# Kernel tuning notes

Hardware: AMD Instinct MI355X
Metric: run time of the kernel (lower is better)

## Reference

```python
import math
import jax, jax.numpy as jnp
import numpy as np

CLUSTER_RATIO1 = 0.0625
CLUSTER_RATIO2 = 0.35
K_LAYER1 = 8
K_LAYER2 = 3


def _dpc_knn(x, cluster_num, k, key):
    """Density-peak clustering with KNN density. x: [B,N,C] -> idx_cluster [B,N]."""
    B, N, C = x.shape
    sq = jnp.sum(x * x, axis=-1)  # [B,N]
    d2 = sq[:, :, None] + sq[:, None, :] - 2.0 * jnp.einsum('bnc,bmc->bnm', x, x)
    dist = jnp.sqrt(jnp.maximum(d2, 0.0)) / jnp.sqrt(jnp.asarray(C, x.dtype))  # cdist / C**0.5
    # k nearest (smallest) distances
    neg_dn, _ = jax.lax.top_k(-dist, k)
    dist_nearest = -neg_dn  # [B,N,k]
    density = jnp.exp(-jnp.mean(dist_nearest ** 2, axis=-1))
    density = density + jax.random.uniform(key, density.shape, dtype=density.dtype) * 1e-6
    mask = (density[:, None, :] > density[:, :, None]).astype(x.dtype)  # [B,N,N]
    dist_max = jnp.max(dist.reshape(B, -1), axis=-1)[:, None, None]
    parent_dist = jnp.min(dist * mask + dist_max * (1.0 - mask), axis=-1)  # [B,N]
    score = parent_dist * density
    _, index_down = jax.lax.top_k(score, cluster_num)  # [B,cluster_num] cluster centers
    # assign each token to nearest center
    dm = jnp.take_along_axis(dist, index_down[:, :, None], axis=1)  # [B,cluster_num,N]
    idx_cluster = jnp.argmin(dm, axis=1)  # [B,N]
    bidx = jnp.arange(B)[:, None]
    idx_cluster = idx_cluster.at[bidx, index_down].set(
        jnp.broadcast_to(jnp.arange(cluster_num)[None, :], index_down.shape))
    return idx_cluster


def _merge_tokens(x, idx_cluster, cluster_num):
    """Weighted (uniform) scatter-mean of tokens into clusters. x: [B,N,C]."""
    B, N, C = x.shape
    flat = (idx_cluster + jnp.arange(B)[:, None] * cluster_num).reshape(-1)  # [B*N]
    ones = jnp.ones((B * N,), x.dtype)
    all_w = jax.ops.segment_sum(ones, flat, num_segments=B * cluster_num) + 1e-6
    norm_w = 1.0 / all_w[flat]  # token_weight == 1
    merged = jax.ops.segment_sum(x.reshape(B * N, C) * norm_w[:, None], flat,
                                 num_segments=B * cluster_num)
    return merged.reshape(B, cluster_num, C)


def _group(meta1, meta2, idx_cluster2, score_w, score_b):
    """Reorder [meta2[v]; members of cluster v from meta1] per cluster, scaled by modulation."""
    T, K1, C = meta1.shape
    K2 = meta2.shape[1]
    modu = jax.nn.softmax(meta2.mean(axis=2) @ score_w.T + score_b, axis=-1)  # [T,K2]
    # composite sort key: (cluster_id, 0 for meta2 center, 1+i for meta1 member i) -> stable grouping
    cid = jnp.concatenate([jnp.broadcast_to(jnp.arange(K2)[None, :], (T, K2)),
                           idx_cluster2], axis=1)  # [T,K2+K1]
    pos = jnp.concatenate([jnp.zeros((T, K2), jnp.int32),
                           jnp.broadcast_to(jnp.arange(1, K1 + 1, dtype=jnp.int32)[None, :], (T, K1))],
                          axis=1)
    sort_key = cid * (K1 + 2) + pos
    order = jnp.argsort(sort_key, axis=1)  # stable; keys are unique anyway
    tokens = jnp.concatenate([meta2, meta1], axis=1)  # [T,K2+K1,C]
    sorted_tokens = jnp.take_along_axis(tokens, order[:, :, None], axis=1)
    sorted_cid = jnp.take_along_axis(cid, order, axis=1)
    scale = jnp.take_along_axis(modu, sorted_cid, axis=1)  # [T,K2+K1]
    return sorted_tokens * scale[:, :, None]


def setup_inputs() -> dict:
    key = jax.random.key(0)
    k1, k2, k3 = jax.random.split(key, 3)
    T, N, C = 128, 256, 1408
    vis_embed = jax.random.normal(k1, (T, N, C), dtype=jnp.float32)
    score_w = jax.random.normal(k2, (6, 6), dtype=jnp.float32) * 0.1
    score_b = jax.random.normal(k3, (6,), dtype=jnp.float32) * 0.1
    return {"vis_embed": vis_embed, "score_w": score_w, "score_b": score_b}


def reference(vis_embed, score_w, score_b):
    T, N, C = vis_embed.shape
    cn1 = max(math.ceil(N * CLUSTER_RATIO1), 1)      # 16
    cn2 = max(math.ceil(cn1 * CLUSTER_RATIO2), 1)    # 6
    nk = jax.random.split(jax.random.key(42), 2)
    idx1 = _dpc_knn(vis_embed, cn1, K_LAYER1, nk[0])
    meta1 = _merge_tokens(vis_embed, idx1, cn1)       # [T,16,C]
    idx2 = _dpc_knn(meta1, cn2, K_LAYER2, nk[1])
    meta2 = _merge_tokens(meta1, idx2, cn2)           # [T,6,C]
    return _group(meta1, meta2, idx2, score_w, score_b)  # [T,22,C]
```

## Files before the change

### kernel.cpp

```cpp
#include <hip/hip_runtime.h>
#include <math.h>

#define T_BATCH 128
#define N_TOK   256
#define C_DIM   1408
#define CN1     16
#define KNN1    8
#define CN2     6
#define KNN2    3
#define NOUT    22
#define LS      44

typedef __attribute__((ext_vector_type(4))) short sh4;
typedef __attribute__((ext_vector_type(8))) short sh8;
typedef __attribute__((ext_vector_type(4))) float f32x4;

union frag_u { sh4 h[2]; sh8 v; };

__device__ inline sh8 ld_frag(const short* p) {
    frag_u u;
    u.h[0] = *(const sh4*)p;
    u.h[1] = *(const sh4*)(p + 4);
    return u.v;
}

__device__ inline void split2(float v0, float v1, unsigned& hip, unsigned& lop) {
    unsigned u0 = __float_as_uint(v0);
    unsigned u1 = __float_as_uint(v1);
    hip = (u0 >> 16) | (u1 & 0xFFFF0000u);
    float l0 = v0 - __uint_as_float(u0 & 0xFFFF0000u);
    float l1 = v1 - __uint_as_float(u1 & 0xFFFF0000u);
    unsigned w0 = __float_as_uint(l0);
    unsigned w1 = __float_as_uint(l1);
    w0 = w0 + 0x7FFFu + ((w0 >> 16) & 1u);
    w1 = w1 + 0x7FFFu + ((w1 >> 16) & 1u);
    lop = (w0 >> 16) | (w1 & 0xFFFF0000u);
}

#define INS8(m, v) {                                   \
    float _x = (v);                                    \
    _Pragma("unroll")                                  \
    for (int _q = 0; _q < 8; _q++) {                   \
        float _lo = fminf(m[_q], _x);                  \
        _x = fmaxf(m[_q], _x);                         \
        m[_q] = _lo;                                   \
    }                                                  \
}

__global__ __launch_bounds__(256, 4) void gemm_dist_sym(const float* __restrict__ x,
                                                        float* __restrict__ dist) {
    const int t = blockIdx.y;
    const int p = blockIdx.x;
    const int bi = (p < 4) ? 0 : (p < 7) ? 1 : (p < 9) ? 2 : 3;
    const int bj = (p < 4) ? p : (p < 7) ? p - 3 : (p < 9) ? p - 5 : 3;
    const int i0 = bi * 64, j0 = bj * 64;
    const bool diag = (bi == bj);
    const float* X = x + (size_t)t * N_TOK * C_DIM;

    __shared__ short Ahi[64 * LS], Alo[64 * LS], Bhi[64 * LS], Blo[64 * LS];
    __shared__ float nred[512];
    __shared__ float snA[64], snB[64];

    const int tid  = threadIdx.x;
    const int wave = tid >> 6;
    const int lane = tid & 63;
    const int qr   = wave >> 1;
    const int qc   = wave & 1;
    const int srow = tid >> 2;
    const int sq   = tid & 3;
    const int fr   = lane & 15;
    const int fq   = lane >> 4;

    const short* BhiS = diag ? Ahi : Bhi;
    const short* BloS = diag ? Alo : Blo;

    f32x4 acc[2][2];
#pragma unroll
    for (int a = 0; a < 2; a++)
#pragma unroll
        for (int b = 0; b < 2; b++) acc[a][b] = (f32x4){0.f, 0.f, 0.f, 0.f};

    const float* Arow = X + (size_t)(i0 + srow) * C_DIM + sq * 8;
    const float* Brow = X + (size_t)(j0 + srow) * C_DIM + sq * 8;
    float nA = 0.f, nB = 0.f;

    for (int k0 = 0; k0 < C_DIM; k0 += 32) {
        float av[8], bv[8];
        float4 a0 = *(const float4*)(Arow + k0);
        float4 a1 = *(const float4*)(Arow + k0 + 4);
        av[0] = a0.x; av[1] = a0.y; av[2] = a0.z; av[3] = a0.w;
        av[4] = a1.x; av[5] = a1.y; av[6] = a1.z; av[7] = a1.w;
#pragma unroll
        for (int e = 0; e < 8; e++) nA += av[e] * av[e];
        unsigned ah[4], al[4], bh[4], bl[4];
#pragma unroll
        for (int q = 0; q < 4; q++) split2(av[2 * q], av[2 * q + 1], ah[q], al[q]);
        if (!diag) {
            float4 b0 = *(const float4*)(Brow + k0);
            float4 b1 = *(const float4*)(Brow + k0 + 4);
            bv[0] = b0.x; bv[1] = b0.y; bv[2] = b0.z; bv[3] = b0.w;
            bv[4] = b1.x; bv[5] = b1.y; bv[6] = b1.z; bv[7] = b1.w;
#pragma unroll
            for (int e = 0; e < 8; e++) nB += bv[e] * bv[e];
#pragma unroll
            for (int q = 0; q < 4; q++) split2(bv[2 * q], bv[2 * q + 1], bh[q], bl[q]);
        }
        __syncthreads();
        {
            unsigned* AH = (unsigned*)&Ahi[srow * LS + sq * 8];
            unsigned* AL = (unsigned*)&Alo[srow * LS + sq * 8];
#pragma unroll
            for (int q = 0; q < 4; q++) { AH[q] = ah[q]; AL[q] = al[q]; }
            if (!diag) {
                unsigned* BH = (unsigned*)&Bhi[srow * LS + sq * 8];
                unsigned* BL = (unsigned*)&Blo[srow * LS + sq * 8];
#pragma unroll
                for (int q = 0; q < 4; q++) { BH[q] = bh[q]; BL[q] = bl[q]; }
            }
        }
        __syncthreads();

        sh8 fAh[2], fAl[2], fBh[2], fBl[2];
#pragma unroll
        for (int mt = 0; mt < 2; mt++) {
            int ro = (qr * 32 + mt * 16 + fr) * LS + fq * 8;
            fAh[mt] = ld_frag(&Ahi[ro]);
            fAl[mt] = ld_frag(&Alo[ro]);
            int co = (qc * 32 + mt * 16 + fr) * LS + fq * 8;
            fBh[mt] = ld_frag(&BhiS[co]);
            fBl[mt] = ld_frag(&BloS[co]);
        }
#pragma unroll
        for (int mt = 0; mt < 2; mt++)
#pragma unroll
            for (int nt = 0; nt < 2; nt++) {
                acc[mt][nt] = __builtin_amdgcn_mfma_f32_16x16x32_bf16(fAh[mt], fBh[nt], acc[mt][nt], 0, 0, 0);
                acc[mt][nt] = __builtin_amdgcn_mfma_f32_16x16x32_bf16(fAh[mt], fBl[nt], acc[mt][nt], 0, 0, 0);
                acc[mt][nt] = __builtin_amdgcn_mfma_f32_16x16x32_bf16(fAl[mt], fBh[nt], acc[mt][nt], 0, 0, 0);
            }
    }

    nred[tid] = nA;
    nred[256 + tid] = diag ? nA : nB;
    __syncthreads();
    if (tid < 64) {
        snA[tid] = nred[4 * tid] + nred[4 * tid + 1] + nred[4 * tid + 2] + nred[4 * tid + 3];
        snB[tid] = nred[256 + 4 * tid] + nred[256 + 4 * tid + 1]
                 + nred[256 + 4 * tid + 2] + nred[256 + 4 * tid + 3];
    }
    __syncthreads();

    const float inv_sqrtC = 1.0f / sqrtf((float)C_DIM);
    float* Dt = dist + (size_t)t * N_TOK * N_TOK;
#pragma unroll
    for (int mt = 0; mt < 2; mt++)
#pragma unroll
        for (int nt = 0; nt < 2; nt++) {
            int jl = qc * 32 + nt * 16 + fr;
            int jg = j0 + jl;
            float sqj = snB[jl];
            int il0 = qr * 32 + mt * 16 + fq * 4;
            float vv[4];
#pragma unroll
            for (int r = 0; r < 4; r++) {
                int ig = i0 + il0 + r;
                float d2 = snA[il0 + r] + sqj - 2.0f * acc[mt][nt][r];
                float v = (ig == jg) ? 0.0f : sqrtf(fmaxf(d2, 0.0f)) * inv_sqrtC;
                Dt[(size_t)ig * N_TOK + jg] = v;
                vv[r] = v;
            }
            if (!diag) {
                float4 o; o.x = vv[0]; o.y = vv[1]; o.z = vv[2]; o.w = vv[3];
                *(float4*)&Dt[(size_t)jg * N_TOK + i0 + il0] = o;
            }
        }
}

__global__ __launch_bounds__(512) void dpc1_fused(const float* __restrict__ dist,
                                                  int* __restrict__ memb,
                                                  int* __restrict__ cntg,
                                                  int* __restrict__ offg) {
    const int t   = blockIdx.x;
    const int tid = threadIdx.x;
    const int col = tid & 255;
    const int h   = tid >> 8;
    const float* D = dist + (size_t)t * N_TOK * N_TOK;

    __shared__ float dens_s[N_TOK];
    __shared__ float red[512];
    __shared__ float lists[KNN1][520];
    __shared__ unsigned long long wbest[8];
    __shared__ int centers[CN1];
    __shared__ int bks[N_TOK];
    __shared__ int cnt_s[CN1], off_s[CN1];

    float c0[8], c1[8], c2[8], c3[8];
#pragma unroll
    for (int q = 0; q < 8; q++) { c0[q] = 3.4e38f; c1[q] = 3.4e38f; c2[q] = 3.4e38f; c3[q] = 3.4e38f; }
    float mx = 0.f;
    const float* base = D + (size_t)(h * 128) * N_TOK + col;
    for (int jj = 0; jj < 128; jj += 4) {
        float d0 = base[(size_t)(jj + 0) * N_TOK];
        float d1 = base[(size_t)(jj + 1) * N_TOK];
        float d2 = base[(size_t)(jj + 2) * N_TOK];
        float d3 = base[(size_t)(jj + 3) * N_TOK];
        mx = fmaxf(mx, fmaxf(fmaxf(d0, d1), fmaxf(d2, d3)));
        INS8(c0, d0); INS8(c1, d1); INS8(c2, d2); INS8(c3, d3);
    }
#pragma unroll
    for (int q = 0; q < 8; q++) { INS8(c0, c1[q]); }
#pragma unroll
    for (int q = 0; q < 8; q++) { INS8(c0, c2[q]); }
#pragma unroll
    for (int q = 0; q < 8; q++) { INS8(c0, c3[q]); }
#pragma unroll
    for (int q = 0; q < 8; q++) lists[q][tid] = c0[q];
    red[tid] = mx;
    __syncthreads();
#pragma unroll
    for (int s = 256; s > 0; s >>= 1) {
        if (tid < s) red[tid] = fmaxf(red[tid], red[tid + s]);
        __syncthreads();
    }
    const float dmax = red[0];
    __syncthreads();

    if (h == 0) {
#pragma unroll
        for (int q = 0; q < 8; q++) { float v = lists[q][col + 256]; INS8(c0, v); }
        float s2 = 0.f;
#pragma unroll
        for (int q = 0; q < 8; q++) s2 += c0[q] * c0[q];
        dens_s[col] = expf(-s2 / (float)KNN1);
    }
    __syncthreads();
    const float dens = dens_s[col];

    float p0 = dmax, p1 = dmax, p2 = dmax, p3 = dmax;
    const float* dsh = dens_s + h * 128;
    for (int jj = 0; jj < 128; jj += 4) {
        float d0 = base[(size_t)(jj + 0) * N_TOK];
        float d1 = base[(size_t)(jj + 1) * N_TOK];
        float d2 = base[(size_t)(jj + 2) * N_TOK];
        float d3 = base[(size_t)(jj + 3) * N_TOK];
        p0 = (dsh[jj + 0] > dens) ? fminf(p0, d0) : p0;
        p1 = (dsh[jj + 1] > dens) ? fminf(p1, d1) : p1;
        p2 = (dsh[jj + 2] > dens) ? fminf(p2, d2) : p2;
        p3 = (dsh[jj + 3] > dens) ? fminf(p3, d3) : p3;
    }
    red[tid] = fminf(fminf(p0, p1), fminf(p2, p3));
    __syncthreads();
    float score = 0.f;
    if (h == 0) score = fminf(red[col], red[col + 256]) * dens;

    unsigned long long key = 0;
    if (h == 0)
        key = ((unsigned long long)__float_as_uint(score) << 32) | (unsigned)(65535 - col);
    for (int k = 0; k < CN1; k++) {
        unsigned long long mm = key;
#pragma unroll
        for (int off = 32; off > 0; off >>= 1) {
            unsigned long long o = __shfl_xor(mm, off);
            mm = (o > mm) ? o : mm;
        }
        if ((tid & 63) == 0) wbest[tid >> 6] = mm;
        __syncthreads();
        unsigned long long b = wbest[0];
#pragma unroll
        for (int w = 1; w < 8; w++) b = (wbest[w] > b) ? wbest[w] : b;
        int idx = 65535 - (int)(b & 0xFFFFull);
        if (tid == 0) centers[k] = idx;
        if (tid == idx) key = 0;
        __syncthreads();
    }

    int bk = 0;
    if (h == 0) {
        float bd = 3.4e38f;
#pragma unroll
        for (int k = 0; k < CN1; k++) {
            float d = D[(size_t)centers[k] * N_TOK + col];
            if (d < bd) { bd = d; bk = k; }
        }
#pragma unroll
        for (int k = 0; k < CN1; k++) if (col == centers[k]) bk = k;
        bks[col] = bk;
    }
    __syncthreads();
    if (tid < CN1) {
        int c = 0;
        for (int j = 0; j < N_TOK; j++) c += (bks[j] == tid);
        cnt_s[tid] = c;
    }
    __syncthreads();
    if (tid == 0) {
        int o = 0;
        for (int q = 0; q < CN1; q++) { off_s[q] = o; o += cnt_s[q]; }
    }
    __syncthreads();
    if (h == 0) {
        int rank = 0;
        for (int j = 0; j < col; j++) rank += (bks[j] == bk);
        memb[t * N_TOK + off_s[bk] + rank] = col;
    }
    if (tid < CN1) {
        cntg[t * CN1 + tid] = cnt_s[tid];
        offg[t * CN1 + tid] = off_s[tid];
    }
}

__global__ __launch_bounds__(256) void merge1_kernel(const float* __restrict__ x,
                                                     const int* __restrict__ memb,
                                                     const int* __restrict__ cntg,
                                                     const int* __restrict__ offg,
                                                     float* __restrict__ meta1) {
    const int q   = blockIdx.x;
    const int t   = blockIdx.y;
    const int tid = threadIdx.x;
    const int n    = cntg[t * CN1 + q];
    const int base = t * N_TOK + offg[t * CN1 + q];
    const int c0 = tid, c1 = tid + 256;
    const bool act1 = (c1 < C_DIM / 4);

    float a0x = 0.f, a0y = 0.f, a0z = 0.f, a0w = 0.f;
    float a1x = 0.f, a1y = 0.f, a1z = 0.f, a1w = 0.f;
    for (int m = 0; m < n; m++) {
        int row = memb[base + m];
        const float4* xr = (const float4*)(x + ((size_t)t * N_TOK + row) * C_DIM);
        float4 v0 = xr[c0];
        a0x += v0.x; a0y += v0.y; a0z += v0.z; a0w += v0.w;
        if (act1) {
            float4 v1 = xr[c1];
            a1x += v1.x; a1y += v1.y; a1z += v1.z; a1w += v1.w;
        }
    }
    float w = 1.0f / ((float)n + 1e-6f);
    float4* mr = (float4*)(meta1 + ((size_t)t * CN1 + q) * C_DIM);
    float4 o0; o0.x = a0x * w; o0.y = a0y * w; o0.z = a0z * w; o0.w = a0w * w;
    mr[c0] = o0;
    if (act1) {
        float4 o1; o1.x = a1x * w; o1.y = a1y * w; o1.z = a1z * w; o1.w = a1w * w;
        mr[c1] = o1;
    }
}

__global__ __launch_bounds__(256) void layer2_kernel(const float* __restrict__ meta1,
                                                     const float* __restrict__ score_w,
                                                     const float* __restrict__ score_b,
                                                     float* __restrict__ out) {
    const int t   = blockIdx.x;
    const int tid = threadIdx.x;
    const float* M = meta1 + (size_t)t * CN1 * C_DIM;

    __shared__ float buf[CN1][132];
    __shared__ float d2s[CN1][CN1];
    __shared__ float m2[CN2][C_DIM];
    __shared__ float dens[CN1], scor[CN1], nrm[CN1], rmx[CN1];
    __shared__ int   centers[CN2], idx2s[CN1], cnt2[CN2];
    __shared__ float modu[CN2], msum[CN2];
    __shared__ int   srcRow[NOUT], cidArr[NOUT];
    __shared__ float dmax_sh;

    const int ti = tid >> 4;
    const int tj = tid & 15;

    float acc = 0.f;
    for (int c0 = 0; c0 < C_DIM; c0 += 128) {
        for (int e = tid; e < CN1 * 128; e += 256) {
            int r = e >> 7, c = e & 127;
            buf[r][c] = M[(size_t)r * C_DIM + c0 + c];
        }
        __syncthreads();
#pragma unroll
        for (int cc = 0; cc < 128; cc += 4) {
            float4 a = *(const float4*)&buf[ti][cc];
            float4 b = *(const float4*)&buf[tj][cc];
            acc += a.x * b.x + a.y * b.y + a.z * b.z + a.w * b.w;
        }
        __syncthreads();
    }
    if (ti == tj) nrm[ti] = acc;
    __syncthreads();

    const float inv_sqrtC = 1.0f / sqrtf((float)C_DIM);
    {
        float d2 = nrm[ti] + nrm[tj] - 2.f * acc;
        d2s[ti][tj] = sqrtf(fmaxf(d2, 0.f)) * inv_sqrtC;
    }
    __syncthreads();

    if (tid < CN1) {
        float m0 = 3.4e38f, m1 = 3.4e38f, m2v = 3.4e38f, mx = 0.f;
        for (int j = 0; j < CN1; j++) {
            float d = d2s[tid][j];
            mx = fmaxf(mx, d);
            if (d < m2v) {
                m2v = d;
                if (m2v < m1) { float tmp = m2v; m2v = m1; m1 = tmp; }
                if (m1 < m0)  { float tmp = m1;  m1 = m0;  m0 = tmp; }
            }
        }
        dens[tid] = expf(-(m0 * m0 + m1 * m1 + m2v * m2v) / (float)KNN2);
        rmx[tid] = mx;
    }
    __syncthreads();
    if (tid == 0) {
        float g = 0.f;
        for (int j = 0; j < CN1; j++) g = fmaxf(g, rmx[j]);
        dmax_sh = g;
    }
    __syncthreads();

    if (tid < CN1) {
        float di = dens[tid];
        float pd = dmax_sh;
        for (int j = 0; j < CN1; j++)
            if (dens[j] > di) pd = fminf(pd, d2s[tid][j]);
        scor[tid] = pd * di;
    }
    __syncthreads();

    if (tid == 0) {
        for (int k = 0; k < CN2; k++) {
            float best = -3.4e38f; int bi = 0;
            for (int j = 0; j < CN1; j++)
                if (scor[j] > best) { best = scor[j]; bi = j; }
            centers[k] = bi;
            scor[bi] = -3.4e38f;
        }
    }
    __syncthreads();

    if (tid < CN1) {
        float bd = 3.4e38f; int bk = 0;
#pragma unroll
        for (int k = 0; k < CN2; k++) {
            float d = d2s[centers[k]][tid];
            if (d < bd) { bd = d; bk = k; }
        }
#pragma unroll
        for (int k = 0; k < CN2; k++) if (tid == centers[k]) bk = k;
        idx2s[tid] = bk;
    }
    __syncthreads();

    if (tid == 0) {
        for (int v = 0; v < CN2; v++) cnt2[v] = 0;
        for (int i = 0; i < CN1; i++) cnt2[idx2s[i]]++;
        int slot = 0;
        for (int v = 0; v < CN2; v++) {
            srcRow[slot] = CN1 + v; cidArr[slot] = v; slot++;
            for (int i = 0; i < CN1; i++)
                if (idx2s[i] == v) { srcRow[slot] = i; cidArr[slot] = v; slot++; }
        }
        for (int v = 0; v < CN2; v++) msum[v] = 0.f;
    }
    __syncthreads();

    float ls[CN2] = {0.f, 0.f, 0.f, 0.f, 0.f, 0.f};
    for (int ch = tid; ch < C_DIM; ch += 256) {
        float a6[CN2] = {0.f, 0.f, 0.f, 0.f, 0.f, 0.f};
        for (int r = 0; r < CN1; r++) {
            float v = M[(size_t)r * C_DIM + ch];
            int c = idx2s[r];
#pragma unroll
            for (int q = 0; q < CN2; q++) a6[q] += (c == q) ? v : 0.f;
        }
#pragma unroll
        for (int q = 0; q < CN2; q++) {
            float mv = a6[q] / ((float)cnt2[q] + 1e-6f);
            m2[q][ch] = mv;
            ls[q] += mv;
        }
    }
#pragma unroll
    for (int q = 0; q < CN2; q++) atomicAdd(&msum[q], ls[q]);
    __syncthreads();

    if (tid == 0) {
        float mean[CN2], lg[CN2];
        for (int v = 0; v < CN2; v++) mean[v] = msum[v] / (float)C_DIM;
        float mxl = -3.4e38f;
        for (int u = 0; u < CN2; u++) {
            float s = score_b[u];
            for (int v = 0; v < CN2; v++) s += mean[v] * score_w[u * CN2 + v];
            lg[u] = s;
            mxl = fmaxf(mxl, s);
        }
        float den = 0.f;
        for (int u = 0; u < CN2; u++) { lg[u] = expf(lg[u] - mxl); den += lg[u]; }
        for (int u = 0; u < CN2; u++) modu[u] = lg[u] / den;
    }
    __syncthreads();

    float* ob = out + (size_t)t * NOUT * C_DIM;
    for (int ch = tid; ch < C_DIM; ch += 256) {
#pragma unroll
        for (int s = 0; s < NOUT; s++) {
            int r = srcRow[s];
            float v = (r < CN1) ? M[(size_t)r * C_DIM + ch] : m2[r - CN1][ch];
            ob[(size_t)s * C_DIM + ch] = v * modu[cidArr[s]];
        }
    }
}

extern "C" void kernel_launch(void* const* d_in, const int* in_sizes, int n_in,
                              void* d_out, int out_size, void* d_ws, size_t ws_size,
                              hipStream_t stream) {
    const float* x  = (const float*)d_in[0];
    const float* sw = (const float*)d_in[1];
    const float* sb = (const float*)d_in[2];
    float* out = (float*)d_out;

    float* ws     = (float*)d_ws;
    float* dist   = ws;
    float* meta1  = dist + (size_t)T_BATCH * N_TOK * N_TOK;
    int*   memb   = (int*)(meta1 + (size_t)T_BATCH * CN1 * C_DIM);
    int*   cntg   = memb + (size_t)T_BATCH * N_TOK;
    int*   offg   = cntg + T_BATCH * CN1;

    gemm_dist_sym<<<dim3(10, T_BATCH), 256, 0, stream>>>(x, dist);
    dpc1_fused<<<T_BATCH, 512, 0, stream>>>(dist, memb, cntg, offg);
    merge1_kernel<<<dim3(CN1, T_BATCH), 256, 0, stream>>>(x, memb, cntg, offg, meta1);
    layer2_kernel<<<T_BATCH, 256, 0, stream>>>(meta1, sw, sb, out);
}
```

Baseline: 443.9 us.

## Remap GEMM block order, widen DPC and layer2 blocks, unroll merge gather

```diff
diff --git a/kernel.cpp b/kernel.cpp
--- a/kernel.cpp
+++ b/kernel.cpp
@@ -49,8 +49,12 @@
 
 __global__ __launch_bounds__(256, 4) void gemm_dist_sym(const float* __restrict__ x,
                                                         float* __restrict__ dist) {
-    const int t = blockIdx.y;
-    const int p = blockIdx.x;
+    const int id = blockIdx.x;
+    const int r  = id & 7;
+    const int q8 = id >> 3;
+    const int p  = q8 % 10;
+    const int tt = q8 / 10;
+    const int t  = tt * 8 + r;
     const int bi = (p < 4) ? 0 : (p < 7) ? 1 : (p < 9) ? 2 : 3;
     const int bj = (p < 4) ? p : (p < 7) ? p - 3 : (p < 9) ? p - 5 : 3;
     const int i0 = bi * 64, j0 = bj * 64;
@@ -162,12 +166,12 @@
             int il0 = qr * 32 + mt * 16 + fq * 4;
             float vv[4];
 #pragma unroll
-            for (int r = 0; r < 4; r++) {
-                int ig = i0 + il0 + r;
-                float d2 = snA[il0 + r] + sqj - 2.0f * acc[mt][nt][r];
+            for (int rr = 0; rr < 4; rr++) {
+                int ig = i0 + il0 + rr;
+                float d2 = snA[il0 + rr] + sqj - 2.0f * acc[mt][nt][rr];
                 float v = (ig == jg) ? 0.0f : sqrtf(fmaxf(d2, 0.0f)) * inv_sqrtC;
                 Dt[(size_t)ig * N_TOK + jg] = v;
-                vv[r] = v;
+                vv[rr] = v;
             }
             if (!diag) {
                 float4 o; o.x = vv[0]; o.y = vv[1]; o.z = vv[2]; o.w = vv[3];
@@ -176,58 +180,55 @@
         }
 }
 
-__global__ __launch_bounds__(512) void dpc1_fused(const float* __restrict__ dist,
-                                                  int* __restrict__ memb,
-                                                  int* __restrict__ cntg,
-                                                  int* __restrict__ offg) {
-    const int t   = blockIdx.x;
-    const int tid = threadIdx.x;
-    const int col = tid & 255;
-    const int h   = tid >> 8;
+__global__ __launch_bounds__(1024) void dpc1_fused(const float* __restrict__ dist,
+                                                   int* __restrict__ memb,
+                                                   int* __restrict__ cntg,
+                                                   int* __restrict__ offg) {
+    const int t    = blockIdx.x;
+    const int tid  = threadIdx.x;
+    const int col  = tid & 255;
+    const int h    = tid >> 8;
+    const int lane = tid & 63;
+    const int wid  = tid >> 6;
     const float* D = dist + (size_t)t * N_TOK * N_TOK;
 
     __shared__ float dens_s[N_TOK];
-    __shared__ float red[512];
-    __shared__ float lists[KNN1][520];
-    __shared__ unsigned long long wbest[8];
+    __shared__ float lists[KNN1][1024];
+    __shared__ float red[1024];
+    __shared__ float rmax16[16];
+    __shared__ unsigned long long wred[16];
     __shared__ int centers[CN1];
     __shared__ int bks[N_TOK];
     __shared__ int cnt_s[CN1], off_s[CN1];
 
-    float c0[8], c1[8], c2[8], c3[8];
-#pragma unroll
-    for (int q = 0; q < 8; q++) { c0[q] = 3.4e38f; c1[q] = 3.4e38f; c2[q] = 3.4e38f; c3[q] = 3.4e38f; }
+    float c0[8], c1[8];
+#pragma unroll
+    for (int q = 0; q < 8; q++) { c0[q] = 3.4e38f; c1[q] = 3.4e38f; }
     float mx = 0.f;
-    const float* base = D + (size_t)(h * 128) * N_TOK + col;
-    for (int jj = 0; jj < 128; jj += 4) {
+    const float* base = D + (size_t)(h * 64) * N_TOK + col;
+    for (int jj = 0; jj < 64; jj += 2) {
         float d0 = base[(size_t)(jj + 0) * N_TOK];
         float d1 = base[(size_t)(jj + 1) * N_TOK];
-        float d2 = base[(size_t)(jj + 2) * N_TOK];
-        float d3 = base[(size_t)(jj + 3) * N_TOK];
-        mx = fmaxf(mx, fmaxf(fmaxf(d0, d1), fmaxf(d2, d3)));
-        INS8(c0, d0); INS8(c1, d1); INS8(c2, d2); INS8(c3, d3);
+        mx = fmaxf(mx, fmaxf(d0, d1));
+        INS8(c0, d0); INS8(c1, d1);
     }
 #pragma unroll
     for (int q = 0; q < 8; q++) { INS8(c0, c1[q]); }
 #pragma unroll
-    for (int q = 0; q < 8; q++) { INS8(c0, c2[q]); }
-#pragma unroll
-    for (int q = 0; q < 8; q++) { INS8(c0, c3[q]); }
-#pragma unroll
     for (int q = 0; q < 8; q++) lists[q][tid] = c0[q];
-    red[tid] = mx;
-    __syncthreads();
-#pragma unroll
-    for (int s = 256; s > 0; s >>= 1) {
-        if (tid < s) red[tid] = fmaxf(red[tid], red[tid + s]);
-        __syncthreads();
-    }
-    const float dmax = red[0];
-    __syncthreads();
+#pragma unroll
+    for (int off = 32; off > 0; off >>= 1) mx = fmaxf(mx, __shfl_xor(mx, off));
+    if (lane == 0) rmax16[wid] = mx;
+    __syncthreads();
+    float dmax = rmax16[0];
+#pragma unroll
+    for (int w = 1; w < 16; w++) dmax = fmaxf(dmax, rmax16[w]);
 
     if (h == 0) {
 #pragma unroll
-        for (int q = 0; q < 8; q++) { float v = lists[q][col + 256]; INS8(c0, v); }
+        for (int s = 1; s < 4; s++)
+#pragma unroll
+            for (int q = 0; q < 8; q++) { float v = lists[q][col + s * 256]; INS8(c0, v); }
         float s2 = 0.f;
 #pragma unroll
         for (int q = 0; q < 8; q++) s2 += c0[q] * c0[q];
@@ -236,22 +237,20 @@
     __syncthreads();
     const float dens = dens_s[col];
 
-    float p0 = dmax, p1 = dmax, p2 = dmax, p3 = dmax;
-    const float* dsh = dens_s + h * 128;
-    for (int jj = 0; jj < 128; jj += 4) {
+    float p0 = dmax, p1 = dmax;
+    const float* dsh = dens_s + h * 64;
+    for (int jj = 0; jj < 64; jj += 2) {
         float d0 = base[(size_t)(jj + 0) * N_TOK];
         float d1 = base[(size_t)(jj + 1) * N_TOK];
-        float d2 = base[(size_t)(jj + 2) * N_TOK];
-        float d3 = base[(size_t)(jj + 3) * N_TOK];
         p0 = (dsh[jj + 0] > dens) ? fminf(p0, d0) : p0;
         p1 = (dsh[jj + 1] > dens) ? fminf(p1, d1) : p1;
-        p2 = (dsh[jj + 2] > dens) ? fminf(p2, d2) : p2;
-        p3 = (dsh[jj + 3] > dens) ? fminf(p3, d3) : p3;
-    }
-    red[tid] = fminf(fminf(p0, p1), fminf(p2, p3));
+    }
+    red[tid] = fminf(p0, p1);
     __syncthreads();
     float score = 0.f;
-    if (h == 0) score = fminf(red[col], red[col + 256]) * dens;
+    if (h == 0)
+        score = fminf(fminf(red[col], red[col + 256]),
+                      fminf(red[col + 512], red[col + 768])) * dens;
 
     unsigned long long key = 0;
     if (h == 0)
@@ -263,11 +262,11 @@
             unsigned long long o = __shfl_xor(mm, off);
             mm = (o > mm) ? o : mm;
         }
-        if ((tid & 63) == 0) wbest[tid >> 6] = mm;
+        if (lane == 0) wred[wid] = mm;
         __syncthreads();
-        unsigned long long b = wbest[0];
-#pragma unroll
-        for (int w = 1; w < 8; w++) b = (wbest[w] > b) ? wbest[w] : b;
+        unsigned long long b = wred[0];
+#pragma unroll
+        for (int w = 1; w < 16; w++) b = (wred[w] > b) ? wred[w] : b;
         int idx = 65535 - (int)(b & 0xFFFFull);
         if (tid == 0) centers[k] = idx;
         if (tid == idx) key = 0;
@@ -321,33 +320,59 @@
     const int base = t * N_TOK + offg[t * CN1 + q];
     const int c0 = tid, c1 = tid + 256;
     const bool act1 = (c1 < C_DIM / 4);
-
-    float a0x = 0.f, a0y = 0.f, a0z = 0.f, a0w = 0.f;
-    float a1x = 0.f, a1y = 0.f, a1z = 0.f, a1w = 0.f;
-    for (int m = 0; m < n; m++) {
-        int row = memb[base + m];
-        const float4* xr = (const float4*)(x + ((size_t)t * N_TOK + row) * C_DIM);
-        float4 v0 = xr[c0];
-        a0x += v0.x; a0y += v0.y; a0z += v0.z; a0w += v0.w;
+    const float4* xb = (const float4*)(x + (size_t)t * N_TOK * C_DIM);
+    const int stride4 = C_DIM / 4;
+
+    float4 s0 = {0.f, 0.f, 0.f, 0.f};
+    float4 s1 = {0.f, 0.f, 0.f, 0.f};
+    int m = 0;
+    for (; m + 4 <= n; m += 4) {
+        int r0 = memb[base + m + 0];
+        int r1 = memb[base + m + 1];
+        int r2 = memb[base + m + 2];
+        int r3 = memb[base + m + 3];
+        float4 a0 = xb[(size_t)r0 * stride4 + c0];
+        float4 a1 = xb[(size_t)r1 * stride4 + c0];
+        float4 a2 = xb[(size_t)r2 * stride4 + c0];
+        float4 a3 = xb[(size_t)r3 * stride4 + c0];
+        s0.x += a0.x; s0.y += a0.y; s0.z += a0.z; s0.w += a0.w;
+        s0.x += a1.x; s0.y += a1.y; s0.z += a1.z; s0.w += a1.w;
+        s0.x += a2.x; s0.y += a2.y; s0.z += a2.z; s0.w += a2.w;
+        s0.x += a3.x; s0.y += a3.y; s0.z += a3.z; s0.w += a3.w;
         if (act1) {
-            float4 v1 = xr[c1];
-            a1x += v1.x; a1y += v1.y; a1z += v1.z; a1w += v1.w;
+            float4 b0 = xb[(size_t)r0 * stride4 + c1];
+            float4 b1 = xb[(size_t)r1 * stride4 + c1];
+            float4 b2 = xb[(size_t)r2 * stride4 + c1];
+            float4 b3 = xb[(size_t)r3 * stride4 + c1];
+            s1.x += b0.x; s1.y += b0.y; s1.z += b0.z; s1.w += b0.w;
+            s1.x += b1.x; s1.y += b1.y; s1.z += b1.z; s1.w += b1.w;
+            s1.x += b2.x; s1.y += b2.y; s1.z += b2.z; s1.w += b2.w;
+            s1.x += b3.x; s1.y += b3.y; s1.z += b3.z; s1.w += b3.w;
+        }
+    }
+    for (; m < n; m++) {
+        int r0 = memb[base + m];
+        float4 a0 = xb[(size_t)r0 * stride4 + c0];
+        s0.x += a0.x; s0.y += a0.y; s0.z += a0.z; s0.w += a0.w;
+        if (act1) {
+            float4 b0 = xb[(size_t)r0 * stride4 + c1];
+            s1.x += b0.x; s1.y += b0.y; s1.z += b0.z; s1.w += b0.w;
         }
     }
     float w = 1.0f / ((float)n + 1e-6f);
     float4* mr = (float4*)(meta1 + ((size_t)t * CN1 + q) * C_DIM);
-    float4 o0; o0.x = a0x * w; o0.y = a0y * w; o0.z = a0z * w; o0.w = a0w * w;
+    float4 o0; o0.x = s0.x * w; o0.y = s0.y * w; o0.z = s0.z * w; o0.w = s0.w * w;
     mr[c0] = o0;
     if (act1) {
-        float4 o1; o1.x = a1x * w; o1.y = a1y * w; o1.z = a1z * w; o1.w = a1w * w;
+        float4 o1; o1.x = s1.x * w; o1.y = s1.y * w; o1.z = s1.z * w; o1.w = s1.w * w;
         mr[c1] = o1;
     }
 }
 
-__global__ __launch_bounds__(256) void layer2_kernel(const float* __restrict__ meta1,
-                                                     const float* __restrict__ score_w,
-                                                     const float* __restrict__ score_b,
-                                                     float* __restrict__ out) {
+__global__ __launch_bounds__(1024) void layer2_kernel(const float* __restrict__ meta1,
+                                                      const float* __restrict__ score_w,
+                                                      const float* __restrict__ score_b,
+                                                      float* __restrict__ out) {
     const int t   = blockIdx.x;
     const int tid = threadIdx.x;
     const float* M = meta1 + (size_t)t * CN1 * C_DIM;
@@ -361,29 +386,31 @@
     __shared__ int   srcRow[NOUT], cidArr[NOUT];
     __shared__ float dmax_sh;
 
-    const int ti = tid >> 4;
+    const int ti = (tid < 256) ? (tid >> 4) : 0;
     const int tj = tid & 15;
 
     float acc = 0.f;
     for (int c0 = 0; c0 < C_DIM; c0 += 128) {
-        for (int e = tid; e < CN1 * 128; e += 256) {
+        for (int e = tid; e < CN1 * 128; e += 1024) {
             int r = e >> 7, c = e & 127;
             buf[r][c] = M[(size_t)r * C_DIM + c0 + c];
         }
         __syncthreads();
-#pragma unroll
-        for (int cc = 0; cc < 128; cc += 4) {
-            float4 a = *(const float4*)&buf[ti][cc];
-            float4 b = *(const float4*)&buf[tj][cc];
-            acc += a.x * b.x + a.y * b.y + a.z * b.z + a.w * b.w;
+        if (tid < 256) {
+#pragma unroll
+            for (int cc = 0; cc < 128; cc += 4) {
+                float4 a = *(const float4*)&buf[ti][cc];
+                float4 b = *(const float4*)&buf[tj][cc];
+                acc += a.x * b.x + a.y * b.y + a.z * b.z + a.w * b.w;
+            }
         }
         __syncthreads();
     }
-    if (ti == tj) nrm[ti] = acc;
+    if (tid < 256 && ti == tj) nrm[ti] = acc;
     __syncthreads();
 
     const float inv_sqrtC = 1.0f / sqrtf((float)C_DIM);
-    {
+    if (tid < 256) {
         float d2 = nrm[ti] + nrm[tj] - 2.f * acc;
         d2s[ti][tj] = sqrtf(fmaxf(d2, 0.f)) * inv_sqrtC;
     }
@@ -458,7 +485,7 @@
     __syncthreads();
 
     float ls[CN2] = {0.f, 0.f, 0.f, 0.f, 0.f, 0.f};
-    for (int ch = tid; ch < C_DIM; ch += 256) {
+    for (int ch = tid; ch < C_DIM; ch += 1024) {
         float a6[CN2] = {0.f, 0.f, 0.f, 0.f, 0.f, 0.f};
         for (int r = 0; r < CN1; r++) {
             float v = M[(size_t)r * C_DIM + ch];
@@ -494,7 +521,7 @@
     __syncthreads();
 
     float* ob = out + (size_t)t * NOUT * C_DIM;
-    for (int ch = tid; ch < C_DIM; ch += 256) {
+    for (int ch = tid; ch < C_DIM; ch += 1024) {
 #pragma unroll
         for (int s = 0; s < NOUT; s++) {
             int r = srcRow[s];
@@ -519,8 +546,8 @@
     int*   cntg   = memb + (size_t)T_BATCH * N_TOK;
     int*   offg   = cntg + T_BATCH * CN1;
 
-    gemm_dist_sym<<<dim3(10, T_BATCH), 256, 0, stream>>>(x, dist);
-    dpc1_fused<<<T_BATCH, 512, 0, stream>>>(dist, memb, cntg, offg);
+    gemm_dist_sym<<<1280, 256, 0, stream>>>(x, dist);
+    dpc1_fused<<<T_BATCH, 1024, 0, stream>>>(dist, memb, cntg, offg);
     merge1_kernel<<<dim3(CN1, T_BATCH), 256, 0, stream>>>(x, memb, cntg, offg, meta1);
-    layer2_kernel<<<T_BATCH, 256, 0, stream>>>(meta1, sw, sb, out);
-}
+    layer2_kernel<<<T_BATCH, 1024, 0, stream>>>(meta1, sw, sb, out);
+}
```

After: 429.8 us. -3.2%, faster.
